# Optimization experiments

Hardware: AMD Instinct MI355X
Metric: run time of the kernel (lower is better)

The kernel has to match this reference:

```python
import jax, jax.numpy as jnp
import numpy as np

SIGMA = 1.0
TOP_K = 4

def setup_inputs() -> dict:
    key = jax.random.key(0)
    k1, k2, k3, k4 = jax.random.split(key, 4)
    B, N, IN_DIM, OUT_DIM, P = 2, 4096, 128, 128, 3
    x = jax.random.normal(k1, (B, N, IN_DIM), dtype=jnp.float32)
    pos = jax.random.normal(k2, (B, N, P), dtype=jnp.float32)
    # Linear(in_dim, out_dim): W [in_dim, out_dim], b [out_dim]
    lim = 1.0 / np.sqrt(IN_DIM)
    W = jax.random.uniform(k3, (IN_DIM, OUT_DIM), minval=-lim, maxval=lim, dtype=jnp.float32)
    b = jax.random.uniform(k4, (OUT_DIM,), minval=-lim, maxval=lim, dtype=jnp.float32)
    return {"x": x, "pos": pos, "W": W, "b": b}

def reference(x, pos, W, b):
    B, N, _ = x.shape
    # pairwise distances [B, N, N]
    pos_diff = pos[:, :, None, :] - pos[:, None, :, :]
    dist = jnp.sqrt(jnp.sum(pos_diff ** 2, axis=-1) + 1e-8)
    adj = jnp.exp(-dist ** 2 / (2.0 * SIGMA ** 2))
    # top-k mask along last dim
    _, indices = jax.lax.top_k(adj, TOP_K)  # [B, N, k]
    b_idx = jnp.arange(B)[:, None, None]
    n_idx = jnp.arange(N)[None, :, None]
    mask = jnp.zeros_like(adj).at[b_idx, n_idx, indices].set(1.0)
    adj = adj * mask
    adj = adj / (jnp.sum(adj, axis=-1, keepdims=True) + 1e-8)
    # weighted aggregation + linear
    out = jnp.einsum('bnm,bmd->bnd', adj, x)
    return out @ W + b
```

## Files before the change

### kernel.cpp

```cpp
#include <hip/hip_runtime.h>
#include <hip/hip_bf16.h>

#define NPTS 4096
#define NROWS 8192
#define DIM 128
#define RPW 2

typedef __attribute__((ext_vector_type(8))) short bf16x8;
typedef __attribute__((ext_vector_type(4))) float f32x4;

__global__ __launch_bounds__(256) void prep(const float* __restrict__ pos,
                                            const float* __restrict__ W,
                                            float4* __restrict__ pos4,
                                            __hip_bfloat16* __restrict__ Wt) {
    int t = blockIdx.x * 256 + threadIdx.x;
    if (t < NROWS) {
        const float* p = pos + (size_t)t * 3;
        pos4[t] = make_float4(p[0], p[1], p[2], 0.f);
    } else if (t < NROWS + DIM * DIM) {
        int i = t - NROWS;
        int n = i >> 7, k = i & 127;
        Wt[i] = __float2bfloat16(W[k * DIM + n]);
    }
}

__global__ __launch_bounds__(256) void xw_mfma(const float* __restrict__ x,
                                               const __hip_bfloat16* __restrict__ Wt,
                                               __hip_bfloat16* __restrict__ xWb) {
    int wave = threadIdx.x >> 6;
    int lane = threadIdx.x & 63;
    int tile = blockIdx.x * 4 + wave;
    int m0 = (tile >> 3) << 4;
    int n0 = (tile & 7) << 4;
    int r = lane & 15;
    int kg = lane >> 4;
    const float* xr = x + (size_t)(m0 + r) * DIM + kg * 8;
    const __hip_bfloat16* br = Wt + (size_t)(n0 + r) * DIM + kg * 8;
    f32x4 acc = {0.f, 0.f, 0.f, 0.f};
#pragma unroll
    for (int kb = 0; kb < 4; ++kb) {
        float4 a0 = *(const float4*)(xr + kb * 32);
        float4 a1 = *(const float4*)(xr + kb * 32 + 4);
        bf16x8 af;
        union { __hip_bfloat16 h; short s; } u;
        u.h = __float2bfloat16(a0.x); af[0] = u.s;
        u.h = __float2bfloat16(a0.y); af[1] = u.s;
        u.h = __float2bfloat16(a0.z); af[2] = u.s;
        u.h = __float2bfloat16(a0.w); af[3] = u.s;
        u.h = __float2bfloat16(a1.x); af[4] = u.s;
        u.h = __float2bfloat16(a1.y); af[5] = u.s;
        u.h = __float2bfloat16(a1.z); af[6] = u.s;
        u.h = __float2bfloat16(a1.w); af[7] = u.s;
        bf16x8 bfr = *(const bf16x8*)(br + kb * 32);
        acc = __builtin_amdgcn_mfma_f32_16x16x32_bf16(af, bfr, acc, 0, 0, 0);
    }
    int col = n0 + r;
    int rbase = m0 + (kg << 2);
#pragma unroll
    for (int reg = 0; reg < 4; ++reg)
        xWb[(size_t)(rbase + reg) * DIM + col] = __float2bfloat16(acc[reg]);
}

__device__ __forceinline__ void ins(float& v0, float& v1, float& v2, float& v3,
                                    int& i0, int& i1, int& i2, int& i3,
                                    float s, int j) {
    bool c3 = s < v3, c2 = s < v2, c1 = s < v1, c0 = s < v0;
    float nv3 = c3 ? (c2 ? v2 : s) : v3;  int n3 = c3 ? (c2 ? i2 : j) : i3;
    float nv2 = c2 ? (c1 ? v1 : s) : v2;  int n2 = c2 ? (c1 ? i1 : j) : i2;
    float nv1 = c1 ? (c0 ? v0 : s) : v1;  int n1 = c1 ? (c0 ? i0 : j) : i1;
    float nv0 = c0 ? s : v0;              int n0 = c0 ? j : i0;
    v3 = nv3; v2 = nv2; v1 = nv1; v0 = nv0;
    i3 = n3;  i2 = n2;  i1 = n1;  i0 = n0;
}

__global__ __launch_bounds__(256) void topk_agg(const float4* __restrict__ pos4,
                                                const __hip_bfloat16* __restrict__ xWb,
                                                const float* __restrict__ bias,
                                                float* __restrict__ out) {
    int lane = threadIdx.x & 63;
    int wave = threadIdx.x >> 6;
    int rowbase = blockIdx.x * (4 * RPW) + wave * RPW;
    int batch = rowbase >> 12;
    int ibase = rowbase & (NPTS - 1);
    const float4* pb = pos4 + (size_t)batch * NPTS;

    float cx[RPW], cy[RPW], cz[RPW];
    float v0[RPW], v1[RPW], v2[RPW], v3[RPW];
    int   i0[RPW], i1[RPW], i2[RPW], i3[RPW];
#pragma unroll
    for (int k = 0; k < RPW; ++k) {
        float4 c = pb[ibase + k];
        cx[k] = c.x; cy[k] = c.y; cz[k] = c.z;
        v0[k] = v1[k] = v2[k] = v3[k] = 3.4e38f;
        i0[k] = i1[k] = i2[k] = i3[k] = 0;
    }

#pragma unroll 2
    for (int j = lane; j < NPTS; j += 64) {
        float4 p = pb[j];
#pragma unroll
        for (int k = 0; k < RPW; ++k) {
            float dx = cx[k] - p.x, dy = cy[k] - p.y, dz = cz[k] - p.z;
            float d2 = fmaf(dx, dx, fmaf(dy, dy, dz * dz));
            ins(v0[k], v1[k], v2[k], v3[k], i0[k], i1[k], i2[k], i3[k], d2, j);
        }
    }

#pragma unroll
    for (int k = 0; k < RPW; ++k) {
        for (int off = 1; off < 64; off <<= 1) {
            float p0 = __shfl_xor(v0[k], off), p1 = __shfl_xor(v1[k], off);
            float p2 = __shfl_xor(v2[k], off), p3 = __shfl_xor(v3[k], off);
            int   q0 = __shfl_xor(i0[k], off), q1 = __shfl_xor(i1[k], off);
            int   q2 = __shfl_xor(i2[k], off), q3 = __shfl_xor(i3[k], off);
            ins(v0[k], v1[k], v2[k], v3[k], i0[k], i1[k], i2[k], i3[k], p0, q0);
            ins(v0[k], v1[k], v2[k], v3[k], i0[k], i1[k], i2[k], i3[k], p1, q1);
            ins(v0[k], v1[k], v2[k], v3[k], i0[k], i1[k], i2[k], i3[k], p2, q2);
            ins(v0[k], v1[k], v2[k], v3[k], i0[k], i1[k], i2[k], i3[k], p3, q3);
        }
    }

    int c = lane << 1;
    float2 bb = *(const float2*)(bias + c);
    const unsigned short* xu = (const unsigned short*)xWb;
    size_t bbase = ((size_t)batch * NPTS) << 7;
#pragma unroll
    for (int k = 0; k < RPW; ++k) {
        float w0 = __expf(-(v0[k] + 1e-8f) * 0.5f);
        float w1 = __expf(-(v1[k] + 1e-8f) * 0.5f);
        float w2 = __expf(-(v2[k] + 1e-8f) * 0.5f);
        float w3 = __expf(-(v3[k] + 1e-8f) * 0.5f);
        float inv = 1.0f / (w0 + w1 + w2 + w3 + 1e-8f);
        w0 *= inv; w1 *= inv; w2 *= inv; w3 *= inv;
        ushort2 a0 = *(const ushort2*)(xu + bbase + ((size_t)i0[k] << 7) + c);
        ushort2 a1 = *(const ushort2*)(xu + bbase + ((size_t)i1[k] << 7) + c);
        ushort2 a2 = *(const ushort2*)(xu + bbase + ((size_t)i2[k] << 7) + c);
        ushort2 a3 = *(const ushort2*)(xu + bbase + ((size_t)i3[k] << 7) + c);
        float ox = bb.x + w0 * __uint_as_float((unsigned)a0.x << 16)
                        + w1 * __uint_as_float((unsigned)a1.x << 16)
                        + w2 * __uint_as_float((unsigned)a2.x << 16)
                        + w3 * __uint_as_float((unsigned)a3.x << 16);
        float oy = bb.y + w0 * __uint_as_float((unsigned)a0.y << 16)
                        + w1 * __uint_as_float((unsigned)a1.y << 16)
                        + w2 * __uint_as_float((unsigned)a2.y << 16)
                        + w3 * __uint_as_float((unsigned)a3.y << 16);
        *(float2*)(out + (((size_t)(rowbase + k)) << 7) + c) = make_float2(ox, oy);
    }
}

extern "C" void kernel_launch(void* const* d_in, const int* in_sizes, int n_in,
                              void* d_out, int out_size, void* d_ws, size_t ws_size,
                              hipStream_t stream) {
    const float* x    = (const float*)d_in[0];
    const float* pos  = (const float*)d_in[1];
    const float* W    = (const float*)d_in[2];
    const float* bias = (const float*)d_in[3];
    float* out = (float*)d_out;

    char* ws = (char*)d_ws;
    __hip_bfloat16* xWb = (__hip_bfloat16*)ws;
    float4* pos4 = (float4*)(ws + (size_t)NROWS * DIM * 2);
    __hip_bfloat16* Wt = (__hip_bfloat16*)(ws + (size_t)NROWS * DIM * 2
                                              + (size_t)NROWS * 16);

    prep<<<(NROWS + DIM * DIM + 255) / 256, 256, 0, stream>>>(pos, W, pos4, Wt);
    xw_mfma<<<(NROWS / 16) * (DIM / 16) / 4, 256, 0, stream>>>(x, Wt, xWb);
    topk_agg<<<NROWS / (4 * RPW), 256, 0, stream>>>(pos4, xWb, bias, out);
}
```

Baseline: 104.5 us.

## Pack distance and index into double keys; split point scan across two waves

Encodes each squared distance and its point index into one double so top-4 insertion and merging use fmin/fmax instead of paired compare/select on values and indices. The cross-lane reduction becomes a bitonic merge of sorted 4-lists. Each row pair's scan is split between two waves and merged through shared memory, doubling the grid. This trades FP64 min/max throughput and an extra block barrier for fewer instructions and more parallelism.

```diff
diff --git a/kernel.cpp b/kernel.cpp
--- a/kernel.cpp
+++ b/kernel.cpp
@@ -4,7 +4,6 @@
 #define NPTS 4096
 #define NROWS 8192
 #define DIM 128
-#define RPW 2
 
 typedef __attribute__((ext_vector_type(8))) short bf16x8;
 typedef __attribute__((ext_vector_type(4))) float f32x4;
@@ -61,16 +60,28 @@
         xWb[(size_t)(rbase + reg) * DIM + col] = __float2bfloat16(acc[reg]);
 }
 
-__device__ __forceinline__ void ins(float& v0, float& v1, float& v2, float& v3,
-                                    int& i0, int& i1, int& i2, int& i3,
-                                    float s, int j) {
-    bool c3 = s < v3, c2 = s < v2, c1 = s < v1, c0 = s < v0;
-    float nv3 = c3 ? (c2 ? v2 : s) : v3;  int n3 = c3 ? (c2 ? i2 : j) : i3;
-    float nv2 = c2 ? (c1 ? v1 : s) : v2;  int n2 = c2 ? (c1 ? i1 : j) : i2;
-    float nv1 = c1 ? (c0 ? v0 : s) : v1;  int n1 = c1 ? (c0 ? i0 : j) : i1;
-    float nv0 = c0 ? s : v0;              int n0 = c0 ? j : i0;
-    v3 = nv3; v2 = nv2; v1 = nv1; v0 = nv0;
-    i3 = n3;  i2 = n2;  i1 = n1;  i0 = n0;
+__device__ __forceinline__ double mkkey(float d2, int j) {
+    return __longlong_as_double(__double_as_longlong((double)d2) |
+                                (unsigned long long)(unsigned)j);
+}
+
+__device__ __forceinline__ void kins(double& k0, double& k1, double& k2,
+                                     double& k3, double s) {
+    double c = fmax(k0, s); k0 = fmin(k0, s);
+    double t = fmax(k1, c); k1 = fmin(k1, c); c = t;
+    t = fmax(k2, c);        k2 = fmin(k2, c); c = t;
+    k3 = fmin(k3, c);
+}
+
+__device__ __forceinline__ void kmerge(double& a0, double& a1, double& a2,
+                                       double& a3, double b0, double b1,
+                                       double b2, double b3) {
+    double m0 = fmin(a0, b3), m1 = fmin(a1, b2);
+    double m2 = fmin(a2, b1), m3 = fmin(a3, b0);
+    double t0 = fmin(m0, m2), t2 = fmax(m0, m2);
+    double t1 = fmin(m1, m3), t3 = fmax(m1, m3);
+    a0 = fmin(t0, t1); a1 = fmax(t0, t1);
+    a2 = fmin(t2, t3); a3 = fmax(t2, t3);
 }
 
 __global__ __launch_bounds__(256) void topk_agg(const float4* __restrict__ pos4,
@@ -79,71 +90,87 @@
                                                 float* __restrict__ out) {
     int lane = threadIdx.x & 63;
     int wave = threadIdx.x >> 6;
-    int rowbase = blockIdx.x * (4 * RPW) + wave * RPW;
+    int group = wave >> 1;
+    int half = wave & 1;
+    int rowbase = blockIdx.x * 4 + group * 2;
     int batch = rowbase >> 12;
     int ibase = rowbase & (NPTS - 1);
     const float4* pb = pos4 + (size_t)batch * NPTS;
 
-    float cx[RPW], cy[RPW], cz[RPW];
-    float v0[RPW], v1[RPW], v2[RPW], v3[RPW];
-    int   i0[RPW], i1[RPW], i2[RPW], i3[RPW];
-#pragma unroll
-    for (int k = 0; k < RPW; ++k) {
-        float4 c = pb[ibase + k];
-        cx[k] = c.x; cy[k] = c.y; cz[k] = c.z;
-        v0[k] = v1[k] = v2[k] = v3[k] = 3.4e38f;
-        i0[k] = i1[k] = i2[k] = i3[k] = 0;
-    }
+    float4 q0 = pb[ibase], q1 = pb[ibase + 1];
+    const double INF = __builtin_inf();
+    double a0 = INF, a1 = INF, a2 = INF, a3 = INF;
+    double b0 = INF, b1 = INF, b2 = INF, b3 = INF;
 
-#pragma unroll 2
-    for (int j = lane; j < NPTS; j += 64) {
+    int jbase = (half << 11) + lane;
+#pragma unroll 4
+    for (int t = 0; t < 32; ++t) {
+        int j = jbase + (t << 6);
         float4 p = pb[j];
-#pragma unroll
-        for (int k = 0; k < RPW; ++k) {
-            float dx = cx[k] - p.x, dy = cy[k] - p.y, dz = cz[k] - p.z;
-            float d2 = fmaf(dx, dx, fmaf(dy, dy, dz * dz));
-            ins(v0[k], v1[k], v2[k], v3[k], i0[k], i1[k], i2[k], i3[k], d2, j);
-        }
+        float dx = q0.x - p.x, dy = q0.y - p.y, dz = q0.z - p.z;
+        float d2 = fmaf(dx, dx, fmaf(dy, dy, dz * dz));
+        kins(a0, a1, a2, a3, mkkey(d2, j));
+        dx = q1.x - p.x; dy = q1.y - p.y; dz = q1.z - p.z;
+        d2 = fmaf(dx, dx, fmaf(dy, dy, dz * dz));
+        kins(b0, b1, b2, b3, mkkey(d2, j));
     }
 
 #pragma unroll
-    for (int k = 0; k < RPW; ++k) {
-        for (int off = 1; off < 64; off <<= 1) {
-            float p0 = __shfl_xor(v0[k], off), p1 = __shfl_xor(v1[k], off);
-            float p2 = __shfl_xor(v2[k], off), p3 = __shfl_xor(v3[k], off);
-            int   q0 = __shfl_xor(i0[k], off), q1 = __shfl_xor(i1[k], off);
-            int   q2 = __shfl_xor(i2[k], off), q3 = __shfl_xor(i3[k], off);
-            ins(v0[k], v1[k], v2[k], v3[k], i0[k], i1[k], i2[k], i3[k], p0, q0);
-            ins(v0[k], v1[k], v2[k], v3[k], i0[k], i1[k], i2[k], i3[k], p1, q1);
-            ins(v0[k], v1[k], v2[k], v3[k], i0[k], i1[k], i2[k], i3[k], p2, q2);
-            ins(v0[k], v1[k], v2[k], v3[k], i0[k], i1[k], i2[k], i3[k], p3, q3);
-        }
+    for (int off = 1; off < 64; off <<= 1) {
+        double p0 = __shfl_xor(a0, off), p1 = __shfl_xor(a1, off);
+        double p2 = __shfl_xor(a2, off), p3 = __shfl_xor(a3, off);
+        kmerge(a0, a1, a2, a3, p0, p1, p2, p3);
+        p0 = __shfl_xor(b0, off); p1 = __shfl_xor(b1, off);
+        p2 = __shfl_xor(b2, off); p3 = __shfl_xor(b3, off);
+        kmerge(b0, b1, b2, b3, p0, p1, p2, p3);
     }
+
+    __shared__ double lds[2][2][2][4];
+    if (lane == 0) {
+        lds[group][half][0][0] = a0; lds[group][half][0][1] = a1;
+        lds[group][half][0][2] = a2; lds[group][half][0][3] = a3;
+        lds[group][half][1][0] = b0; lds[group][half][1][1] = b1;
+        lds[group][half][1][2] = b2; lds[group][half][1][3] = b3;
+    }
+    __syncthreads();
+    if (half) return;
+
+    kmerge(a0, a1, a2, a3, lds[group][1][0][0], lds[group][1][0][1],
+                           lds[group][1][0][2], lds[group][1][0][3]);
+    kmerge(b0, b1, b2, b3, lds[group][1][1][0], lds[group][1][1][1],
+                           lds[group][1][1][2], lds[group][1][1][3]);
 
     int c = lane << 1;
     float2 bb = *(const float2*)(bias + c);
     const unsigned short* xu = (const unsigned short*)xWb;
     size_t bbase = ((size_t)batch * NPTS) << 7;
 #pragma unroll
-    for (int k = 0; k < RPW; ++k) {
-        float w0 = __expf(-(v0[k] + 1e-8f) * 0.5f);
-        float w1 = __expf(-(v1[k] + 1e-8f) * 0.5f);
-        float w2 = __expf(-(v2[k] + 1e-8f) * 0.5f);
-        float w3 = __expf(-(v3[k] + 1e-8f) * 0.5f);
+    for (int k = 0; k < 2; ++k) {
+        double k0 = k ? b0 : a0, k1 = k ? b1 : a1;
+        double k2 = k ? b2 : a2, k3 = k ? b3 : a3;
+        unsigned i0 = (unsigned)__double_as_longlong(k0) & 0xFFFu;
+        unsigned i1 = (unsigned)__double_as_longlong(k1) & 0xFFFu;
+        unsigned i2 = (unsigned)__double_as_longlong(k2) & 0xFFFu;
+        unsigned i3 = (unsigned)__double_as_longlong(k3) & 0xFFFu;
+        float d0 = (float)k0, d1 = (float)k1, d2 = (float)k2, d3 = (float)k3;
+        float w0 = __expf(-(d0 + 1e-8f) * 0.5f);
+        float w1 = __expf(-(d1 + 1e-8f) * 0.5f);
+        float w2 = __expf(-(d2 + 1e-8f) * 0.5f);
+        float w3 = __expf(-(d3 + 1e-8f) * 0.5f);
         float inv = 1.0f / (w0 + w1 + w2 + w3 + 1e-8f);
         w0 *= inv; w1 *= inv; w2 *= inv; w3 *= inv;
-        ushort2 a0 = *(const ushort2*)(xu + bbase + ((size_t)i0[k] << 7) + c);
-        ushort2 a1 = *(const ushort2*)(xu + bbase + ((size_t)i1[k] << 7) + c);
-        ushort2 a2 = *(const ushort2*)(xu + bbase + ((size_t)i2[k] << 7) + c);
-        ushort2 a3 = *(const ushort2*)(xu + bbase + ((size_t)i3[k] << 7) + c);
-        float ox = bb.x + w0 * __uint_as_float((unsigned)a0.x << 16)
-                        + w1 * __uint_as_float((unsigned)a1.x << 16)
-                        + w2 * __uint_as_float((unsigned)a2.x << 16)
-                        + w3 * __uint_as_float((unsigned)a3.x << 16);
-        float oy = bb.y + w0 * __uint_as_float((unsigned)a0.y << 16)
-                        + w1 * __uint_as_float((unsigned)a1.y << 16)
-                        + w2 * __uint_as_float((unsigned)a2.y << 16)
-                        + w3 * __uint_as_float((unsigned)a3.y << 16);
+        ushort2 g0 = *(const ushort2*)(xu + bbase + ((size_t)i0 << 7) + c);
+        ushort2 g1 = *(const ushort2*)(xu + bbase + ((size_t)i1 << 7) + c);
+        ushort2 g2 = *(const ushort2*)(xu + bbase + ((size_t)i2 << 7) + c);
+        ushort2 g3 = *(const ushort2*)(xu + bbase + ((size_t)i3 << 7) + c);
+        float ox = bb.x + w0 * __uint_as_float((unsigned)g0.x << 16)
+                        + w1 * __uint_as_float((unsigned)g1.x << 16)
+                        + w2 * __uint_as_float((unsigned)g2.x << 16)
+                        + w3 * __uint_as_float((unsigned)g3.x << 16);
+        float oy = bb.y + w0 * __uint_as_float((unsigned)g0.y << 16)
+                        + w1 * __uint_as_float((unsigned)g1.y << 16)
+                        + w2 * __uint_as_float((unsigned)g2.y << 16)
+                        + w3 * __uint_as_float((unsigned)g3.y << 16);
         *(float2*)(out + (((size_t)(rowbase + k)) << 7) + c) = make_float2(ox, oy);
     }
 }
@@ -165,5 +192,5 @@
 
     prep<<<(NROWS + DIM * DIM + 255) / 256, 256, 0, stream>>>(pos, W, pos4, Wt);
     xw_mfma<<<(NROWS / 16) * (DIM / 16) / 4, 256, 0, stream>>>(x, Wt, xWb);
-    topk_agg<<<NROWS / (4 * RPW), 256, 0, stream>>>(pos4, xWb, bias, out);
+    topk_agg<<<NROWS / 4, 256, 0, stream>>>(pos4, xWb, bias, out);
 }
```

Result: faster. 91.36 us (-12.5%).
